# Optimization experiments

Hardware: AMD Instinct MI355X
Metric: run time of the kernel (lower is better)

## Reference

```python
import jax, jax.numpy as jnp
import numpy as np

FEAT = 32          # feat_size
N = FEAT * FEAT    # sequence length = 1024
D = 256            # d_model
DK = 32            # per-head dim (hardcoded in module)
H = D // DK        # num_heads = 8
B = 16
NUM_REL = (2 * FEAT - 1) ** 2


def _rel_index():
    coords = np.stack(np.meshgrid(np.arange(FEAT), np.arange(FEAT), indexing='ij'), axis=-1).reshape(-1, 2)
    rel = coords[:, None, :] - coords[None, :, :]  # [N, N, 2]
    rel += FEAT - 1
    return (rel[..., 0] * (2 * FEAT - 1) + rel[..., 1]).astype(np.int32)  # [N, N]


def setup_inputs() -> dict:
    key = jax.random.key(0)
    ks = jax.random.split(key, 10)
    std = 0.02
    inp = {
        'x': jax.random.normal(ks[0], (B, N, D), jnp.float32),
        'Wq': jax.random.normal(ks[1], (D, D), jnp.float32) * std,
        'bq': jnp.zeros((D,), jnp.float32),
        'Wk': jax.random.normal(ks[2], (D, D), jnp.float32) * std,
        'bk': jnp.zeros((D,), jnp.float32),
        'Wv': jax.random.normal(ks[3], (D, D), jnp.float32) * std,
        'bv': jnp.zeros((D,), jnp.float32),
        'Wo': jax.random.normal(ks[4], (D, D), jnp.float32) * std,
        'bo': jnp.zeros((D,), jnp.float32),
        'bias_table': jax.random.normal(ks[5], (H, NUM_REL), jnp.float32) * std,
        'rel_index': jnp.asarray(_rel_index()),  # [N, N] int32
    }
    return inp


def reference(x, Wq, bq, Wk, bk, Wv, bv, Wo, bo, bias_table, rel_index):
    Bn, Nn, C = x.shape
    # torch Linear: y = x @ W.T + b
    def proj(W, b):
        return (x @ W.T + b).reshape(Bn, Nn, H, DK).transpose(0, 2, 1, 3)  # [B,H,N,dk]
    q, k, v = proj(Wq, bq), proj(Wk, bk), proj(Wv, bv)
    # relative position bias gather: [H, N*N] -> [1,H,N,N]
    rel_bias = bias_table[:, rel_index.reshape(-1)].reshape(1, H, Nn, Nn)
    scale = 1.0 / jnp.sqrt(jnp.float32(DK))
    scores = jnp.einsum('bhqd,bhkd->bhqk', q, k) * scale + rel_bias
    attn = jax.nn.softmax(scores, axis=-1)
    out = jnp.einsum('bhqk,bhkd->bhqd', attn, v)  # [B,H,N,dk]
    out = out.transpose(0, 2, 1, 3).reshape(Bn, Nn, C)
    return out @ Wo.T + bo
```

## Files before the change

### kernel.cpp

```cpp
#include <hip/hip_runtime.h>


typedef unsigned short u16;
typedef unsigned int u32;
typedef short short8 __attribute__((ext_vector_type(8)));
typedef u16 u16x4 __attribute__((ext_vector_type(4)));
typedef u32 u32x2 __attribute__((ext_vector_type(2)));
typedef float f32x4 __attribute__((ext_vector_type(4)));

#define NREL 3969
#define LOG2E 1.4426950408889634f
#define QS2 (0.17677669529663687f * 1.4426950408889634f)

__device__ __forceinline__ u16 f2bf(float f) {
  union { float f; unsigned u; } x; x.f = f;
  unsigned r = x.u + 0x7fffu + ((x.u >> 16) & 1u);
  return (u16)(r >> 16);
}

__device__ __forceinline__ u32 cvt_pk_bf16(float lo, float hi) {
  u32 r;
  asm("v_cvt_pk_bf16_f32 %0, %1, %2" : "=v"(r) : "v"(lo), "v"(hi));
  return r;
}

__device__ __forceinline__ float fast_exp2(float x) {
  float r;
  asm("v_exp_f32 %0, %1" : "=v"(r) : "v"(x));
  return r;
}

__device__ __forceinline__ void glds16(const u16* g, u16* l) {
  __builtin_amdgcn_global_load_lds((const __attribute__((address_space(1))) u32*)g,
                                   (__attribute__((address_space(3))) u32*)l, 16, 0, 0);
}

template <int N> __device__ __forceinline__ void wait_vm() {
  asm volatile("s_waitcnt vmcnt(%0)" ::"n"(N) : "memory");
}

__global__ __launch_bounds__(256) void cast_all_k(
    const float4* __restrict__ x,
    const float* __restrict__ wq, const float* __restrict__ wk,
    const float* __restrict__ wv, const float* __restrict__ wo,
    u16x4* __restrict__ xout, u16x4* __restrict__ wout) {
  int i = blockIdx.x * 256 + threadIdx.x;
  float4 v;
  u16x4* dst;
  if (i < 1048576) {
    v = x[i];
    dst = xout + i;
  } else {
    int wf = i - 1048576;
    int wi = wf >> 14, off = wf & 16383;
    const float* src = (wi == 0) ? wq : (wi == 1) ? wk : (wi == 2) ? wv : wo;
    v = ((const float4*)src)[off];
    dst = wout + wf;
  }
  u16x4 o;
  o[0] = f2bf(v.x); o[1] = f2bf(v.y); o[2] = f2bf(v.z); o[3] = f2bf(v.w);
  *dst = o;
}

__global__ __launch_bounds__(256, 3) void proj_qkv_k(
    const u16* __restrict__ A, const u16* __restrict__ Wc,
    const float* __restrict__ b0, const float* __restrict__ b1,
    const float* __restrict__ b2,
    u16* __restrict__ qb, u16* __restrict__ kb, u16* __restrict__ vtb) {
  const int lid = (blockIdx.x & 7) * 96 + (blockIdx.x >> 3);
  const int m0 = (lid / 6) * 128;
  const int n0 = (lid % 6) * 128;
  __shared__ u16 SH[24576];
  const int tid = threadIdx.x;
  const int wave = tid >> 6, lane = tid & 63;
  const int fr = lane & 15, kg = lane >> 4;
  const int wm = wave >> 1, wn = wave & 1;
  const int l2 = lane >> 2;
  const int sseg = ((lane & 3) ^ (l2 & 3)) * 8;
  const u16* gA = A + (m0 + wave * 16 + l2) * 256 + sseg;
  const u16* gB = Wc + (n0 + wave * 16 + l2) * 256 + sseg;
  const int dstw = wave * 1024;
  const int rsw = (kg * 16) ^ ((fr & 3) << 4);

  f32x4 acc[4][4];
#pragma unroll
  for (int i = 0; i < 4; ++i)
#pragma unroll
    for (int j = 0; j < 4; ++j) acc[i][j] = (f32x4){0.f, 0.f, 0.f, 0.f};

  const int ws = (n0 + wn * 64) >> 8;
  const bool vm = (ws == 2);

#define PSTG(t, sb)                                                     \
  do {                                                                  \
    glds16(gA + (t) * 32,         (u16*)((char*)SH + (sb) + dstw));     \
    glds16(gA + 16384 + (t) * 32, (u16*)((char*)SH + (sb) + 4096 + dstw)); \
    glds16(gB + (t) * 32,         (u16*)((char*)SH + (sb) + 8192 + dstw)); \
    glds16(gB + 16384 + (t) * 32, (u16*)((char*)SH + (sb) + 12288 + dstw)); \
  } while (0)

  PSTG(0, 0);
  PSTG(1, 16384);
#pragma unroll
  for (int it = 0; it < 8; ++it) {
    if (it < 6) PSTG(it + 2, ((it + 2) % 3) * 16384);
    if (it < 6) wait_vm<8>();
    else if (it == 6) wait_vm<4>();
    else wait_vm<0>();
    __builtin_amdgcn_s_barrier();
    const char* abase = (const char*)SH + (it % 3) * 16384;
    const char* bbase = abase + 8192;
    short8 af[4], bf[4];
#pragma unroll
    for (int i = 0; i < 4; ++i) {
      af[i] = *(const short8*)(abase + (wm * 64 + i * 16 + fr) * 64 + rsw);
      bf[i] = *(const short8*)(bbase + (wn * 64 + i * 16 + fr) * 64 + rsw);
    }
    if (vm) {
#pragma unroll
      for (int mi = 0; mi < 4; ++mi)
#pragma unroll
        for (int ni = 0; ni < 4; ++ni)
          acc[mi][ni] = __builtin_amdgcn_mfma_f32_16x16x32_bf16(af[mi], bf[ni], acc[mi][ni], 0, 0, 0);
    } else {
#pragma unroll
      for (int mi = 0; mi < 4; ++mi)
#pragma unroll
        for (int ni = 0; ni < 4; ++ni)
          acc[mi][ni] = __builtin_amdgcn_mfma_f32_16x16x32_bf16(bf[ni], af[mi], acc[mi][ni], 0, 0, 0);
    }
    __builtin_amdgcn_s_barrier();
  }
#undef PSTG

  const int bI = m0 >> 10;
  const int s0 = (m0 & 1023) + wm * 64;
  const int nbb = (n0 + wn * 64) & 255;
  char* shw = (char*)SH + wave * 8192;
  if (vm) {
#pragma unroll
    for (int ni = 0; ni < 4; ++ni) {
      const int nl = ni * 16 + fr;
      const float bias = b2[nbb + nl];
#pragma unroll
      for (int mi = 0; mi < 4; ++mi) {
        u16x4 pk;
#pragma unroll
        for (int r = 0; r < 4; ++r) pk[r] = f2bf(acc[mi][ni][r] + bias);
        *(u16x4*)(shw + nl * 128 + (((mi * 16 + kg * 4) * 2) ^ ((nl & 7) << 4))) = pk;
      }
    }
    const int l8 = lane >> 3, seg8 = lane & 7;
#pragma unroll
    for (int i = 0; i < 8; ++i) {
      const int nl = i * 8 + l8;
      const short8 val = *(const short8*)(shw + nl * 128 + ((seg8 * 16) ^ ((nl & 7) << 4)));
      const int hg = (nbb >> 5) + (nl >> 5), dd = nl & 31;
      *(short8*)(vtb + ((bI * 8 + hg) * 32 + dd) * 1024 + s0 + seg8 * 8) = val;
    }
  } else {
    const float* bp = (ws == 0) ? b0 : b1;
    u16* dst = (ws == 0) ? qb : kb;
    const float sc = (ws == 0) ? QS2 : 1.0f;
#pragma unroll
    for (int ni = 0; ni < 4; ++ni) {
      const float4 b4 = *(const float4*)(bp + nbb + ni * 16 + kg * 4);
#pragma unroll
      for (int mi = 0; mi < 4; ++mi) {
        const int sl = mi * 16 + fr;
        u16x4 pk;
#pragma unroll
        for (int r = 0; r < 4; ++r) pk[r] = f2bf((acc[mi][ni][r] + b4[r]) * sc);
        *(u16x4*)(shw + sl * 128 + (((ni * 32 + kg * 8)) ^ ((sl & 7) << 4))) = pk;
      }
    }
    const int l4 = lane >> 2, seg = lane & 3;
#pragma unroll
    for (int hh = 0; hh < 2; ++hh) {
#pragma unroll
      for (int g = 0; g < 4; ++g) {
        const int sl = g * 16 + l4;
        const short8 val = *(const short8*)(shw + sl * 128 + ((hh * 64 + seg * 16) ^ ((sl & 7) << 4)));
        const int hg = (nbb >> 5) + hh;
        *(short8*)(dst + ((bI * 8 + hg) * 1024 + s0 + sl) * 32 + seg * 8) = val;
      }
    }
  }
}

__global__ __launch_bounds__(256, 4) void proj_out_k(
    const u16* __restrict__ A, const u16* __restrict__ Wc,
    const float* __restrict__ bo, float* __restrict__ outp) {
  const int lid = (blockIdx.x & 7) * 64 + (blockIdx.x >> 3);
  const int m0 = (lid >> 1) * 64;
  const int n0 = (lid & 1) * 128;
  __shared__ u16 SH[18432];
  const int tid = threadIdx.x;
  const int wave = tid >> 6, lane = tid & 63;
  const int fr = lane & 15, kg = lane >> 4;
  const int wm = wave >> 1, wn = wave & 1;
  const int l2 = lane >> 2;
  const int sseg = ((lane & 3) ^ (l2 & 3)) * 8;
  const u16* gA = A + (m0 + wave * 16 + l2) * 256 + sseg;
  const u16* gB = Wc + (768 + n0 + wave * 16 + l2) * 256 + sseg;
  const int dstw = wave * 1024;
  const int rsw = (kg * 16) ^ ((fr & 3) << 4);

  f32x4 acc[2][4];
#pragma unroll
  for (int i = 0; i < 2; ++i)
#pragma unroll
    for (int j = 0; j < 4; ++j) acc[i][j] = (f32x4){0.f, 0.f, 0.f, 0.f};

#define OSTG(t, sb)                                                     \
  do {                                                                  \
    glds16(gA + (t) * 32,         (u16*)((char*)SH + (sb) + dstw));     \
    glds16(gB + (t) * 32,         (u16*)((char*)SH + (sb) + 4096 + dstw)); \
    glds16(gB + 16384 + (t) * 32, (u16*)((char*)SH + (sb) + 8192 + dstw)); \
  } while (0)

  OSTG(0, 0);
  OSTG(1, 12288);
#pragma unroll
  for (int it = 0; it < 8; ++it) {
    if (it < 6) OSTG(it + 2, ((it + 2) % 3) * 12288);
    if (it < 6) wait_vm<6>();
    else if (it == 6) wait_vm<3>();
    else wait_vm<0>();
    __builtin_amdgcn_s_barrier();
    const char* abase = (const char*)SH + (it % 3) * 12288;
    const char* bbase = abase + 4096;
    short8 af[2], bf[4];
#pragma unroll
    for (int i = 0; i < 2; ++i)
      af[i] = *(const short8*)(abase + (wm * 32 + i * 16 + fr) * 64 + rsw);
#pragma unroll
    for (int i = 0; i < 4; ++i)
      bf[i] = *(const short8*)(bbase + (wn * 64 + i * 16 + fr) * 64 + rsw);
#pragma unroll
    for (int mi = 0; mi < 2; ++mi)
#pragma unroll
      for (int ni = 0; ni < 4; ++ni)
        acc[mi][ni] = __builtin_amdgcn_mfma_f32_16x16x32_bf16(bf[ni], af[mi], acc[mi][ni], 0, 0, 0);
    __builtin_amdgcn_s_barrier();
  }
#undef OSTG

#pragma unroll
  for (int ni = 0; ni < 4; ++ni) {
    const int n4 = n0 + wn * 64 + ni * 16 + kg * 4;
    const float4 b4 = *(const float4*)(bo + n4);
#pragma unroll
    for (int mi = 0; mi < 2; ++mi) {
      const int m = m0 + wm * 32 + mi * 16 + fr;
      float4 o;
#pragma unroll
      for (int r = 0; r < 4; ++r) o[r] = acc[mi][ni][r] + b4[r];
      *(float4*)(outp + m * 256 + n4) = o;
    }
  }
}

__global__ __launch_bounds__(256, 5) void rel_attn_k(
    const u16* __restrict__ qb, const u16* __restrict__ kb,
    const u16* __restrict__ vtb, const float* __restrict__ btab,
    u16* __restrict__ ao) {
  const int bid0 = blockIdx.x;
  const int lid = (bid0 & 7) * 256 + (bid0 >> 3);
  const int bh = lid >> 4, qt = lid & 15;
  const int h = bh & 7, b = bh >> 3;
  const int q0 = qt * 64;
  __shared__ u16 bias_lb[3972];
  __shared__ u16 Kl[2][2048];
  __shared__ u16 Vl[2][2048];
  __shared__ u16 Pl[4][1024];
  const int tid = threadIdx.x;
  const int wave = tid >> 6, lane = tid & 63;
  const int fr = lane & 15, kg = lane >> 4;

  for (int i = tid; i < NREL; i += 256) bias_lb[i] = f2bf(btab[h * NREL + i] * LOG2E);

  const int krow = tid >> 2;
  const u16* kgsrc = kb + (bh * 1024 + krow) * 32 + ((tid & 3) ^ (krow & 3)) * 8;
  const int vrow = tid >> 3;
  const u16* vgsrc = vtb + (bh * 32 + vrow) * 1024 + ((tid & 7) ^ (vrow & 7)) * 8;
  u16* kld = &Kl[0][0] + wave * 512;
  u16* vld = &Vl[0][0] + wave * 512;

  const int q = q0 + wave * 16 + fr;
  const short8 qf = *(const short8*)(qb + (bh * 1024 + q) * 32 + kg * 8);
  const int qbase = (q >> 5) * 63 + (q & 31) + 1984;
  char* pw = (char*)Pl[wave] + fr * 128;
  const int swz = (fr & 7) << 4;

  short8 ones;
#pragma unroll
  for (int j = 0; j < 8; ++j) ones[j] = (short)0x3F80;

  f32x4 oacc[2], lacc;
  oacc[0] = (f32x4){0.f, 0.f, 0.f, 0.f};
  oacc[1] = (f32x4){0.f, 0.f, 0.f, 0.f};
  lacc = (f32x4){0.f, 0.f, 0.f, 0.f};

  glds16(kgsrc, kld);
  glds16(vgsrc, vld);
  __syncthreads();

  for (int kt = 0; kt < 16; ++kt) {
    const int cur = kt & 1;
    if (kt < 15) {
      glds16(kgsrc + (kt + 1) * 2048, kld + (cur ^ 1) * 2048);
      glds16(vgsrc + (kt + 1) * 64, vld + (cur ^ 1) * 2048);
      wait_vm<2>();
    } else {
      wait_vm<0>();
    }
    __builtin_amdgcn_s_barrier();

    const char* kbase = (const char*)Kl[cur];
    const char* vbase = (const char*)Vl[cur];
    short8 kf[4], vf[2][2];
#pragma unroll
    for (int g = 0; g < 4; ++g)
      kf[g] = *(const short8*)(kbase + (g * 16 + fr) * 64 + ((kg * 16) ^ ((fr & 3) << 4)));
#pragma unroll
    for (int ks = 0; ks < 2; ++ks)
#pragma unroll
      for (int g2 = 0; g2 < 2; ++g2)
        vf[ks][g2] = *(const short8*)(vbase + (g2 * 16 + fr) * 128 + (((ks * 4 + kg) << 4) ^ swz));

    f32x4 sacc[4];
    __builtin_amdgcn_s_setprio(1);
#pragma unroll
    for (int g = 0; g < 4; ++g)
      sacc[g] = __builtin_amdgcn_mfma_f32_16x16x32_bf16(kf[g], qf, (f32x4){0.f, 0.f, 0.f, 0.f}, 0, 0, 0);
    __builtin_amdgcn_s_setprio(0);

    const int t0 = qbase - kt * 126 - kg * 4;
    u32 pk[4][2];
#pragma unroll
    for (int g = 0; g < 4; ++g) {
      const int ag = t0 - g * 16 - 31 * (g >> 1);
      float e[4];
#pragma unroll
      for (int r = 0; r < 4; ++r) {
        union { u32 u; float f; } bc;
        bc.u = (u32)bias_lb[ag - r] << 16;
        e[r] = fast_exp2(sacc[g][r] + bc.f);
      }
      pk[g][0] = cvt_pk_bf16(e[0], e[1]);
      pk[g][1] = cvt_pk_bf16(e[2], e[3]);
    }

#pragma unroll
    for (int g = 0; g < 4; ++g) {
      u32x2 w2;
      w2[0] = pk[g][0];
      w2[1] = pk[g][1];
      *(u32x2*)(pw + ((g * 32 + kg * 8) ^ swz)) = w2;
    }

#pragma unroll
    for (int ks = 0; ks < 2; ++ks) {
      const short8 pf = *(const short8*)(pw + ((ks * 64 + kg * 16) ^ swz));
      __builtin_amdgcn_s_setprio(1);
      oacc[0] = __builtin_amdgcn_mfma_f32_16x16x32_bf16(pf, vf[ks][0], oacc[0], 0, 0, 0);
      oacc[1] = __builtin_amdgcn_mfma_f32_16x16x32_bf16(pf, vf[ks][1], oacc[1], 0, 0, 0);
      lacc = __builtin_amdgcn_mfma_f32_16x16x32_bf16(pf, ones, lacc, 0, 0, 0);
      __builtin_amdgcn_s_setprio(0);
    }
    __builtin_amdgcn_s_barrier();
  }

#pragma unroll
  for (int r = 0; r < 4; ++r) {
    const float inv = __builtin_amdgcn_rcpf(lacc[r]);
#pragma unroll
    for (int g2 = 0; g2 < 2; ++g2)
      *(u16*)((char*)Pl[wave] + (kg * 4 + r) * 64 + (g2 * 16 + fr) * 2) =
          f2bf(oacc[g2][r] * inv);
  }
  const int orow = lane >> 2, oseg = lane & 3;
  const short8 ov = *(const short8*)((char*)Pl[wave] + orow * 64 + oseg * 16);
  *(short8*)(ao + (b * 1024 + q0 + wave * 16 + orow) * 256 + h * 32 + oseg * 8) = ov;
}

extern "C" void kernel_launch(void* const* d_in, const int* in_sizes, int n_in,
                              void* d_out, int out_size, void* d_ws, size_t ws_size,
                              hipStream_t stream) {
  (void)in_sizes; (void)n_in; (void)out_size; (void)ws_size;
  const float* x    = (const float*)d_in[0];
  const float* Wq   = (const float*)d_in[1];
  const float* bq   = (const float*)d_in[2];
  const float* Wk   = (const float*)d_in[3];
  const float* bk   = (const float*)d_in[4];
  const float* Wv   = (const float*)d_in[5];
  const float* bv   = (const float*)d_in[6];
  const float* Wo   = (const float*)d_in[7];
  const float* bo   = (const float*)d_in[8];
  const float* btab = (const float*)d_in[9];
  float* out = (float*)d_out;
  char* ws = (char*)d_ws;

  u16* xbf  = (u16*)(ws + 0);
  u16* Wcat = (u16*)(ws + 8388608);
  u16* qbuf = (u16*)(ws + 8912896);
  u16* kbuf = (u16*)(ws + 17301504);
  u16* vtb  = (u16*)(ws + 25690112);

  cast_all_k<<<4352, 256, 0, stream>>>((const float4*)x, Wq, Wk, Wv, Wo,
                                       (u16x4*)xbf, (u16x4*)Wcat);
  proj_qkv_k<<<768, 256, 0, stream>>>(xbf, Wcat, bq, bk, bv, qbuf, kbuf, vtb);
  rel_attn_k<<<2048, 256, 0, stream>>>(qbuf, kbuf, vtb, btab, xbf);
  proj_out_k<<<512, 256, 0, stream>>>(xbf, Wcat, bo, out);
}
```

Measured before the change: 158.6 us.

## Fuse fp32-to-bf16 cast of x into QKV projection GEMM loads

The separate cast kernel now converts only the weights. The QKV projection reads fp32 x directly, converts it to bf16 in registers and stores it swizzled into LDS, so the bf16 copy of x is no longer written to and read back from HBM. Both projection GEMMs also move from a 3-stage async pipeline to a 2-stage double buffer with __syncthreads, which frees LDS for higher occupancy (launch bound 3→4 for QKV). In exchange the main loop loads A through registers synchronously, which can expose more latency, and the 6 column tiles per row block each re-read fp32 x, which is twice the bytes of bf16.

```diff
diff --git a/kernel.cpp b/kernel.cpp
--- a/kernel.cpp
+++ b/kernel.cpp
@@ -6,6 +6,7 @@
 typedef short short8 __attribute__((ext_vector_type(8)));
 typedef u16 u16x4 __attribute__((ext_vector_type(4)));
 typedef u32 u32x2 __attribute__((ext_vector_type(2)));
+typedef u32 u32x4 __attribute__((ext_vector_type(4)));
 typedef float f32x4 __attribute__((ext_vector_type(4)));
 
 #define NREL 3969
@@ -39,47 +40,39 @@
   asm volatile("s_waitcnt vmcnt(%0)" ::"n"(N) : "memory");
 }
 
-__global__ __launch_bounds__(256) void cast_all_k(
-    const float4* __restrict__ x,
+__global__ __launch_bounds__(256) void cast_w_k(
     const float* __restrict__ wq, const float* __restrict__ wk,
     const float* __restrict__ wv, const float* __restrict__ wo,
-    u16x4* __restrict__ xout, u16x4* __restrict__ wout) {
+    u16x4* __restrict__ wout) {
   int i = blockIdx.x * 256 + threadIdx.x;
-  float4 v;
-  u16x4* dst;
-  if (i < 1048576) {
-    v = x[i];
-    dst = xout + i;
-  } else {
-    int wf = i - 1048576;
-    int wi = wf >> 14, off = wf & 16383;
-    const float* src = (wi == 0) ? wq : (wi == 1) ? wk : (wi == 2) ? wv : wo;
-    v = ((const float4*)src)[off];
-    dst = wout + wf;
-  }
+  int wi = i >> 14, off = i & 16383;
+  const float* src = (wi == 0) ? wq : (wi == 1) ? wk : (wi == 2) ? wv : wo;
+  float4 v = ((const float4*)src)[off];
   u16x4 o;
   o[0] = f2bf(v.x); o[1] = f2bf(v.y); o[2] = f2bf(v.z); o[3] = f2bf(v.w);
-  *dst = o;
-}
-
-__global__ __launch_bounds__(256, 3) void proj_qkv_k(
-    const u16* __restrict__ A, const u16* __restrict__ Wc,
+  wout[i] = o;
+}
+
+__global__ __launch_bounds__(256, 4) void proj_qkv_k(
+    const float* __restrict__ X, const u16* __restrict__ Wc,
     const float* __restrict__ b0, const float* __restrict__ b1,
     const float* __restrict__ b2,
     u16* __restrict__ qb, u16* __restrict__ kb, u16* __restrict__ vtb) {
   const int lid = (blockIdx.x & 7) * 96 + (blockIdx.x >> 3);
   const int m0 = (lid / 6) * 128;
   const int n0 = (lid % 6) * 128;
-  __shared__ u16 SH[24576];
+  __shared__ u16 SH[16384];
   const int tid = threadIdx.x;
   const int wave = tid >> 6, lane = tid & 63;
   const int fr = lane & 15, kg = lane >> 4;
   const int wm = wave >> 1, wn = wave & 1;
   const int l2 = lane >> 2;
   const int sseg = ((lane & 3) ^ (l2 & 3)) * 8;
-  const u16* gA = A + (m0 + wave * 16 + l2) * 256 + sseg;
   const u16* gB = Wc + (n0 + wave * 16 + l2) * 256 + sseg;
-  const int dstw = wave * 1024;
+  const float* gX = X + (m0 + (tid >> 1)) * 256 + (tid & 1) * 16;
+  const int arow = tid >> 1, acg = tid & 1;
+  const int aw0 = arow * 64 + ((acg * 32) ^ ((arow & 3) << 4));
+  const int aw1 = arow * 64 + ((acg * 32 + 16) ^ ((arow & 3) << 4));
   const int rsw = (kg * 16) ^ ((fr & 3) << 4);
 
   f32x4 acc[4][4];
@@ -91,24 +84,33 @@
   const int ws = (n0 + wn * 64) >> 8;
   const bool vm = (ws == 2);
 
-#define PSTG(t, sb)                                                     \
-  do {                                                                  \
-    glds16(gA + (t) * 32,         (u16*)((char*)SH + (sb) + dstw));     \
-    glds16(gA + 16384 + (t) * 32, (u16*)((char*)SH + (sb) + 4096 + dstw)); \
-    glds16(gB + (t) * 32,         (u16*)((char*)SH + (sb) + 8192 + dstw)); \
-    glds16(gB + 16384 + (t) * 32, (u16*)((char*)SH + (sb) + 12288 + dstw)); \
-  } while (0)
-
-  PSTG(0, 0);
-  PSTG(1, 16384);
-#pragma unroll
+  float4 ar[4];
+#pragma unroll
+  for (int q = 0; q < 4; ++q) ar[q] = *(const float4*)(gX + q * 4);
+  glds16(gB, (u16*)((char*)SH + 8192 + wave * 1024));
+  glds16(gB + 16384, (u16*)((char*)SH + 12288 + wave * 1024));
+  {
+    u32x4 w0, w1;
+    w0[0] = cvt_pk_bf16(ar[0][0], ar[0][1]); w0[1] = cvt_pk_bf16(ar[0][2], ar[0][3]);
+    w0[2] = cvt_pk_bf16(ar[1][0], ar[1][1]); w0[3] = cvt_pk_bf16(ar[1][2], ar[1][3]);
+    w1[0] = cvt_pk_bf16(ar[2][0], ar[2][1]); w1[1] = cvt_pk_bf16(ar[2][2], ar[2][3]);
+    w1[2] = cvt_pk_bf16(ar[3][0], ar[3][1]); w1[3] = cvt_pk_bf16(ar[3][2], ar[3][3]);
+    *(u32x4*)((char*)SH + aw0) = w0;
+    *(u32x4*)((char*)SH + aw1) = w1;
+  }
+  __syncthreads();
+
   for (int it = 0; it < 8; ++it) {
-    if (it < 6) PSTG(it + 2, ((it + 2) % 3) * 16384);
-    if (it < 6) wait_vm<8>();
-    else if (it == 6) wait_vm<4>();
-    else wait_vm<0>();
-    __builtin_amdgcn_s_barrier();
-    const char* abase = (const char*)SH + (it % 3) * 16384;
+    const int cb = (it & 1) ? 16384 : 0;
+    const int nb = 16384 - cb;
+    if (it < 7) {
+      const int ko = (it + 1) * 32;
+#pragma unroll
+      for (int q = 0; q < 4; ++q) ar[q] = *(const float4*)(gX + ko + q * 4);
+      glds16(gB + ko, (u16*)((char*)SH + nb + 8192 + wave * 1024));
+      glds16(gB + 16384 + ko, (u16*)((char*)SH + nb + 12288 + wave * 1024));
+    }
+    const char* abase = (const char*)SH + cb;
     const char* bbase = abase + 8192;
     short8 af[4], bf[4];
 #pragma unroll
@@ -129,9 +131,17 @@
         for (int ni = 0; ni < 4; ++ni)
           acc[mi][ni] = __builtin_amdgcn_mfma_f32_16x16x32_bf16(bf[ni], af[mi], acc[mi][ni], 0, 0, 0);
     }
-    __builtin_amdgcn_s_barrier();
-  }
-#undef PSTG
+    if (it < 7) {
+      u32x4 w0, w1;
+      w0[0] = cvt_pk_bf16(ar[0][0], ar[0][1]); w0[1] = cvt_pk_bf16(ar[0][2], ar[0][3]);
+      w0[2] = cvt_pk_bf16(ar[1][0], ar[1][1]); w0[3] = cvt_pk_bf16(ar[1][2], ar[1][3]);
+      w1[0] = cvt_pk_bf16(ar[2][0], ar[2][1]); w1[1] = cvt_pk_bf16(ar[2][2], ar[2][3]);
+      w1[2] = cvt_pk_bf16(ar[3][0], ar[3][1]); w1[3] = cvt_pk_bf16(ar[3][2], ar[3][3]);
+      *(u32x4*)((char*)SH + nb + aw0) = w0;
+      *(u32x4*)((char*)SH + nb + aw1) = w1;
+    }
+    __syncthreads();
+  }
 
   const int bI = m0 >> 10;
   const int s0 = (m0 & 1023) + wm * 64;
@@ -194,7 +204,7 @@
   const int lid = (blockIdx.x & 7) * 64 + (blockIdx.x >> 3);
   const int m0 = (lid >> 1) * 64;
   const int n0 = (lid & 1) * 128;
-  __shared__ u16 SH[18432];
+  __shared__ u16 SH[12288];
   const int tid = threadIdx.x;
   const int wave = tid >> 6, lane = tid & 63;
   const int fr = lane & 15, kg = lane >> 4;
@@ -203,7 +213,6 @@
   const int sseg = ((lane & 3) ^ (l2 & 3)) * 8;
   const u16* gA = A + (m0 + wave * 16 + l2) * 256 + sseg;
   const u16* gB = Wc + (768 + n0 + wave * 16 + l2) * 256 + sseg;
-  const int dstw = wave * 1024;
   const int rsw = (kg * 16) ^ ((fr & 3) << 4);
 
   f32x4 acc[2][4];
@@ -212,23 +221,20 @@
 #pragma unroll
     for (int j = 0; j < 4; ++j) acc[i][j] = (f32x4){0.f, 0.f, 0.f, 0.f};
 
-#define OSTG(t, sb)                                                     \
-  do {                                                                  \
-    glds16(gA + (t) * 32,         (u16*)((char*)SH + (sb) + dstw));     \
-    glds16(gB + (t) * 32,         (u16*)((char*)SH + (sb) + 4096 + dstw)); \
-    glds16(gB + 16384 + (t) * 32, (u16*)((char*)SH + (sb) + 8192 + dstw)); \
+#define OSTG(t, sb)                                                        \
+  do {                                                                     \
+    glds16(gA + (t) * 32,         (u16*)((char*)SH + (sb) + wave * 1024)); \
+    glds16(gB + (t) * 32,         (u16*)((char*)SH + (sb) + 4096 + wave * 1024)); \
+    glds16(gB + 16384 + (t) * 32, (u16*)((char*)SH + (sb) + 8192 + wave * 1024)); \
   } while (0)
 
   OSTG(0, 0);
-  OSTG(1, 12288);
-#pragma unroll
+  __syncthreads();
   for (int it = 0; it < 8; ++it) {
-    if (it < 6) OSTG(it + 2, ((it + 2) % 3) * 12288);
-    if (it < 6) wait_vm<6>();
-    else if (it == 6) wait_vm<3>();
-    else wait_vm<0>();
-    __builtin_amdgcn_s_barrier();
-    const char* abase = (const char*)SH + (it % 3) * 12288;
+    const int cb = (it & 1) ? 12288 : 0;
+    const int nb = 12288 - cb;
+    if (it < 7) OSTG(it + 1, nb);
+    const char* abase = (const char*)SH + cb;
     const char* bbase = abase + 4096;
     short8 af[2], bf[4];
 #pragma unroll
@@ -242,7 +248,7 @@
 #pragma unroll
       for (int ni = 0; ni < 4; ++ni)
         acc[mi][ni] = __builtin_amdgcn_mfma_f32_16x16x32_bf16(bf[ni], af[mi], acc[mi][ni], 0, 0, 0);
-    __builtin_amdgcn_s_barrier();
+    __syncthreads();
   }
 #undef OSTG
 
@@ -402,15 +408,14 @@
   float* out = (float*)d_out;
   char* ws = (char*)d_ws;
 
-  u16* xbf  = (u16*)(ws + 0);
+  u16* abf  = (u16*)(ws + 0);
   u16* Wcat = (u16*)(ws + 8388608);
   u16* qbuf = (u16*)(ws + 8912896);
   u16* kbuf = (u16*)(ws + 17301504);
   u16* vtb  = (u16*)(ws + 25690112);
 
-  cast_all_k<<<4352, 256, 0, stream>>>((const float4*)x, Wq, Wk, Wv, Wo,
-                                       (u16x4*)xbf, (u16x4*)Wcat);
-  proj_qkv_k<<<768, 256, 0, stream>>>(xbf, Wcat, bq, bk, bv, qbuf, kbuf, vtb);
-  rel_attn_k<<<2048, 256, 0, stream>>>(qbuf, kbuf, vtb, btab, xbf);
-  proj_out_k<<<512, 256, 0, stream>>>(xbf, Wcat, bo, out);
-}
+  cast_w_k<<<256, 256, 0, stream>>>(Wq, Wk, Wv, Wo, (u16x4*)Wcat);
+  proj_qkv_k<<<768, 256, 0, stream>>>(x, Wcat, bq, bk, bv, qbuf, kbuf, vtb);
+  rel_attn_k<<<2048, 256, 0, stream>>>(qbuf, kbuf, vtb, btab, abf);
+  proj_out_k<<<512, 256, 0, stream>>>(abf, Wcat, bo, out);
+}
```

After: 224.5 us. +41.6%, slower.

## Process two query tiles per attention block to reuse K/V loads

Applied to the files above, without the earlier changes.

Each attention block now handles 128 query rows (two 64-row sub-tiles per wave) instead of 64, halving the grid to 1024 blocks. K/V tiles and the per-head bias table loaded into LDS are reused across both sub-tiles, which halves global K/V traffic and the bias table setup per query. The cost is more live registers (two sets of accumulators and Q fragments), possibly lower occupancy, and fewer blocks for load balancing.

```diff
diff --git a/kernel.cpp b/kernel.cpp
--- a/kernel.cpp
+++ b/kernel.cpp
@@ -266,10 +266,10 @@
     const u16* __restrict__ vtb, const float* __restrict__ btab,
     u16* __restrict__ ao) {
   const int bid0 = blockIdx.x;
-  const int lid = (bid0 & 7) * 256 + (bid0 >> 3);
-  const int bh = lid >> 4, qt = lid & 15;
+  const int lid = (bid0 & 7) * 128 + (bid0 >> 3);
+  const int bh = lid >> 3, qp = lid & 7;
   const int h = bh & 7, b = bh >> 3;
-  const int q0 = qt * 64;
+  const int q0 = qp * 128;
   __shared__ u16 bias_lb[3972];
   __shared__ u16 Kl[2][2048];
   __shared__ u16 Vl[2][2048];
@@ -287,9 +287,11 @@
   u16* kld = &Kl[0][0] + wave * 512;
   u16* vld = &Vl[0][0] + wave * 512;
 
-  const int q = q0 + wave * 16 + fr;
-  const short8 qf = *(const short8*)(qb + (bh * 1024 + q) * 32 + kg * 8);
-  const int qbase = (q >> 5) * 63 + (q & 31) + 1984;
+  const int qA = q0 + wave * 16 + fr;
+  const short8 qfA = *(const short8*)(qb + (bh * 1024 + qA) * 32 + kg * 8);
+  const short8 qfB = *(const short8*)(qb + (bh * 1024 + qA + 64) * 32 + kg * 8);
+  const int qbaseA = (qA >> 5) * 63 + (qA & 31) + 1984;
+  const int qbaseB = qbaseA + 126;
   char* pw = (char*)Pl[wave] + fr * 128;
   const int swz = (fr & 7) << 4;
 
@@ -297,10 +299,13 @@
 #pragma unroll
   for (int j = 0; j < 8; ++j) ones[j] = (short)0x3F80;
 
-  f32x4 oacc[2], lacc;
-  oacc[0] = (f32x4){0.f, 0.f, 0.f, 0.f};
-  oacc[1] = (f32x4){0.f, 0.f, 0.f, 0.f};
-  lacc = (f32x4){0.f, 0.f, 0.f, 0.f};
+  f32x4 oaccA[2], oaccB[2], laccA, laccB;
+  oaccA[0] = (f32x4){0.f, 0.f, 0.f, 0.f};
+  oaccA[1] = (f32x4){0.f, 0.f, 0.f, 0.f};
+  oaccB[0] = (f32x4){0.f, 0.f, 0.f, 0.f};
+  oaccB[1] = (f32x4){0.f, 0.f, 0.f, 0.f};
+  laccA = (f32x4){0.f, 0.f, 0.f, 0.f};
+  laccB = (f32x4){0.f, 0.f, 0.f, 0.f};
 
   glds16(kgsrc, kld);
   glds16(vgsrc, vld);
@@ -329,60 +334,115 @@
       for (int g2 = 0; g2 < 2; ++g2)
         vf[ks][g2] = *(const short8*)(vbase + (g2 * 16 + fr) * 128 + (((ks * 4 + kg) << 4) ^ swz));
 
-    f32x4 sacc[4];
-    __builtin_amdgcn_s_setprio(1);
-#pragma unroll
-    for (int g = 0; g < 4; ++g)
-      sacc[g] = __builtin_amdgcn_mfma_f32_16x16x32_bf16(kf[g], qf, (f32x4){0.f, 0.f, 0.f, 0.f}, 0, 0, 0);
-    __builtin_amdgcn_s_setprio(0);
-
-    const int t0 = qbase - kt * 126 - kg * 4;
-    u32 pk[4][2];
-#pragma unroll
-    for (int g = 0; g < 4; ++g) {
-      const int ag = t0 - g * 16 - 31 * (g >> 1);
-      float e[4];
-#pragma unroll
-      for (int r = 0; r < 4; ++r) {
-        union { u32 u; float f; } bc;
-        bc.u = (u32)bias_lb[ag - r] << 16;
-        e[r] = fast_exp2(sacc[g][r] + bc.f);
-      }
-      pk[g][0] = cvt_pk_bf16(e[0], e[1]);
-      pk[g][1] = cvt_pk_bf16(e[2], e[3]);
-    }
-
-#pragma unroll
-    for (int g = 0; g < 4; ++g) {
-      u32x2 w2;
-      w2[0] = pk[g][0];
-      w2[1] = pk[g][1];
-      *(u32x2*)(pw + ((g * 32 + kg * 8) ^ swz)) = w2;
-    }
-
-#pragma unroll
-    for (int ks = 0; ks < 2; ++ks) {
-      const short8 pf = *(const short8*)(pw + ((ks * 64 + kg * 16) ^ swz));
+    const int t0k = -kt * 126 - kg * 4;
+
+    {
+      f32x4 sacc[4];
       __builtin_amdgcn_s_setprio(1);
-      oacc[0] = __builtin_amdgcn_mfma_f32_16x16x32_bf16(pf, vf[ks][0], oacc[0], 0, 0, 0);
-      oacc[1] = __builtin_amdgcn_mfma_f32_16x16x32_bf16(pf, vf[ks][1], oacc[1], 0, 0, 0);
-      lacc = __builtin_amdgcn_mfma_f32_16x16x32_bf16(pf, ones, lacc, 0, 0, 0);
+#pragma unroll
+      for (int g = 0; g < 4; ++g)
+        sacc[g] = __builtin_amdgcn_mfma_f32_16x16x32_bf16(kf[g], qfA, (f32x4){0.f, 0.f, 0.f, 0.f}, 0, 0, 0);
       __builtin_amdgcn_s_setprio(0);
-    }
-    __builtin_amdgcn_s_barrier();
-  }
-
+      const int t0 = qbaseA + t0k;
+      u32 pk[4][2];
+#pragma unroll
+      for (int g = 0; g < 4; ++g) {
+        const int ag = t0 - g * 16 - 31 * (g >> 1);
+        float e[4];
+#pragma unroll
+        for (int r = 0; r < 4; ++r) {
+          union { u32 u; float f; } bc;
+          bc.u = (u32)bias_lb[ag - r] << 16;
+          e[r] = fast_exp2(sacc[g][r] + bc.f);
+        }
+        pk[g][0] = cvt_pk_bf16(e[0], e[1]);
+        pk[g][1] = cvt_pk_bf16(e[2], e[3]);
+      }
+#pragma unroll
+      for (int g = 0; g < 4; ++g) {
+        u32x2 w2;
+        w2[0] = pk[g][0];
+        w2[1] = pk[g][1];
+        *(u32x2*)(pw + ((g * 32 + kg * 8) ^ swz)) = w2;
+      }
+#pragma unroll
+      for (int ks = 0; ks < 2; ++ks) {
+        const short8 pf = *(const short8*)(pw + ((ks * 64 + kg * 16) ^ swz));
+        __builtin_amdgcn_s_setprio(1);
+        oaccA[0] = __builtin_amdgcn_mfma_f32_16x16x32_bf16(pf, vf[ks][0], oaccA[0], 0, 0, 0);
+        oaccA[1] = __builtin_amdgcn_mfma_f32_16x16x32_bf16(pf, vf[ks][1], oaccA[1], 0, 0, 0);
+        laccA = __builtin_amdgcn_mfma_f32_16x16x32_bf16(pf, ones, laccA, 0, 0, 0);
+        __builtin_amdgcn_s_setprio(0);
+      }
+    }
+
+    {
+      f32x4 sacc[4];
+      __builtin_amdgcn_s_setprio(1);
+#pragma unroll
+      for (int g = 0; g < 4; ++g)
+        sacc[g] = __builtin_amdgcn_mfma_f32_16x16x32_bf16(kf[g], qfB, (f32x4){0.f, 0.f, 0.f, 0.f}, 0, 0, 0);
+      __builtin_amdgcn_s_setprio(0);
+      const int t0 = qbaseB + t0k;
+      u32 pk[4][2];
+#pragma unroll
+      for (int g = 0; g < 4; ++g) {
+        const int ag = t0 - g * 16 - 31 * (g >> 1);
+        float e[4];
+#pragma unroll
+        for (int r = 0; r < 4; ++r) {
+          union { u32 u; float f; } bc;
+          bc.u = (u32)bias_lb[ag - r] << 16;
+          e[r] = fast_exp2(sacc[g][r] + bc.f);
+        }
+        pk[g][0] = cvt_pk_bf16(e[0], e[1]);
+        pk[g][1] = cvt_pk_bf16(e[2], e[3]);
+      }
+#pragma unroll
+      for (int g = 0; g < 4; ++g) {
+        u32x2 w2;
+        w2[0] = pk[g][0];
+        w2[1] = pk[g][1];
+        *(u32x2*)(pw + ((g * 32 + kg * 8) ^ swz)) = w2;
+      }
+#pragma unroll
+      for (int ks = 0; ks < 2; ++ks) {
+        const short8 pf = *(const short8*)(pw + ((ks * 64 + kg * 16) ^ swz));
+        __builtin_amdgcn_s_setprio(1);
+        oaccB[0] = __builtin_amdgcn_mfma_f32_16x16x32_bf16(pf, vf[ks][0], oaccB[0], 0, 0, 0);
+        oaccB[1] = __builtin_amdgcn_mfma_f32_16x16x32_bf16(pf, vf[ks][1], oaccB[1], 0, 0, 0);
+        laccB = __builtin_amdgcn_mfma_f32_16x16x32_bf16(pf, ones, laccB, 0, 0, 0);
+        __builtin_amdgcn_s_setprio(0);
+      }
+    }
+    __builtin_amdgcn_s_barrier();
+  }
+
+  const int orow = lane >> 2, oseg = lane & 3;
 #pragma unroll
   for (int r = 0; r < 4; ++r) {
-    const float inv = __builtin_amdgcn_rcpf(lacc[r]);
+    const float inv = __builtin_amdgcn_rcpf(laccA[r]);
 #pragma unroll
     for (int g2 = 0; g2 < 2; ++g2)
       *(u16*)((char*)Pl[wave] + (kg * 4 + r) * 64 + (g2 * 16 + fr) * 2) =
-          f2bf(oacc[g2][r] * inv);
-  }
-  const int orow = lane >> 2, oseg = lane & 3;
-  const short8 ov = *(const short8*)((char*)Pl[wave] + orow * 64 + oseg * 16);
-  *(short8*)(ao + (b * 1024 + q0 + wave * 16 + orow) * 256 + h * 32 + oseg * 8) = ov;
+          f2bf(oaccA[g2][r] * inv);
+  }
+  {
+    const short8 ov = *(const short8*)((char*)Pl[wave] + orow * 64 + oseg * 16);
+    *(short8*)(ao + (b * 1024 + q0 + wave * 16 + orow) * 256 + h * 32 + oseg * 8) = ov;
+  }
+#pragma unroll
+  for (int r = 0; r < 4; ++r) {
+    const float inv = __builtin_amdgcn_rcpf(laccB[r]);
+#pragma unroll
+    for (int g2 = 0; g2 < 2; ++g2)
+      *(u16*)((char*)Pl[wave] + (kg * 4 + r) * 64 + (g2 * 16 + fr) * 2) =
+          f2bf(oaccB[g2][r] * inv);
+  }
+  {
+    const short8 ov = *(const short8*)((char*)Pl[wave] + orow * 64 + oseg * 16);
+    *(short8*)(ao + (b * 1024 + q0 + 64 + wave * 16 + orow) * 256 + h * 32 + oseg * 8) = ov;
+  }
 }
 
 extern "C" void kernel_launch(void* const* d_in, const int* in_sizes, int n_in,
@@ -411,6 +471,6 @@
   cast_all_k<<<4352, 256, 0, stream>>>((const float4*)x, Wq, Wk, Wv, Wo,
                                        (u16x4*)xbf, (u16x4*)Wcat);
   proj_qkv_k<<<768, 256, 0, stream>>>(xbf, Wcat, bq, bk, bv, qbuf, kbuf, vtb);
-  rel_attn_k<<<2048, 256, 0, stream>>>(qbuf, kbuf, vtb, btab, xbf);
+  rel_attn_k<<<1024, 256, 0, stream>>>(qbuf, kbuf, vtb, btab, xbf);
   proj_out_k<<<512, 256, 0, stream>>>(xbf, Wcat, bo, out);
 }
```

Measured after the change: 166.0 us. 1.05x slower.

## Load K/V fragments directly from global into registers, dropping LDS staging

Applied to the files above, without the earlier changes.

The attention kernel no longer stages K and V tiles through double-buffered shared memory with per-tile barriers. Each wave now loads its MFMA fragments straight from global memory into registers, ping-ponging between two register sets so the next tile's loads overlap the current tile's compute. This removes the LDS traffic and the block-wide barriers, but each of the four waves now fetches the same K/V data separately (more global/L2 traffic) and register pressure rises. The occupancy hint is lowered from 5 to 4 blocks to make room for the extra registers.

```diff
diff --git a/kernel.cpp b/kernel.cpp
--- a/kernel.cpp
+++ b/kernel.cpp
@@ -261,7 +261,7 @@
   }
 }
 
-__global__ __launch_bounds__(256, 5) void rel_attn_k(
+__global__ __launch_bounds__(256, 4) void rel_attn_k(
     const u16* __restrict__ qb, const u16* __restrict__ kb,
     const u16* __restrict__ vtb, const float* __restrict__ btab,
     u16* __restrict__ ao) {
@@ -271,8 +271,6 @@
   const int h = bh & 7, b = bh >> 3;
   const int q0 = qt * 64;
   __shared__ u16 bias_lb[3972];
-  __shared__ u16 Kl[2][2048];
-  __shared__ u16 Vl[2][2048];
   __shared__ u16 Pl[4][1024];
   const int tid = threadIdx.x;
   const int wave = tid >> 6, lane = tid & 63;
@@ -280,16 +278,11 @@
 
   for (int i = tid; i < NREL; i += 256) bias_lb[i] = f2bf(btab[h * NREL + i] * LOG2E);
 
-  const int krow = tid >> 2;
-  const u16* kgsrc = kb + (bh * 1024 + krow) * 32 + ((tid & 3) ^ (krow & 3)) * 8;
-  const int vrow = tid >> 3;
-  const u16* vgsrc = vtb + (bh * 32 + vrow) * 1024 + ((tid & 7) ^ (vrow & 7)) * 8;
-  u16* kld = &Kl[0][0] + wave * 512;
-  u16* vld = &Vl[0][0] + wave * 512;
-
   const int q = q0 + wave * 16 + fr;
   const short8 qf = *(const short8*)(qb + (bh * 1024 + q) * 32 + kg * 8);
   const int qbase = (q >> 5) * 63 + (q & 31) + 1984;
+  const u16* kp = kb + (bh * 1024 + fr) * 32 + kg * 8;
+  const u16* vp = vtb + (bh * 32 + fr) * 1024 + kg * 8;
   char* pw = (char*)Pl[wave] + fr * 128;
   const int swz = (fr & 7) << 4;
 
@@ -302,75 +295,80 @@
   oacc[1] = (f32x4){0.f, 0.f, 0.f, 0.f};
   lacc = (f32x4){0.f, 0.f, 0.f, 0.f};
 
-  glds16(kgsrc, kld);
-  glds16(vgsrc, vld);
   __syncthreads();
 
-  for (int kt = 0; kt < 16; ++kt) {
-    const int cur = kt & 1;
-    if (kt < 15) {
-      glds16(kgsrc + (kt + 1) * 2048, kld + (cur ^ 1) * 2048);
-      glds16(vgsrc + (kt + 1) * 64, vld + (cur ^ 1) * 2048);
-      wait_vm<2>();
-    } else {
-      wait_vm<0>();
-    }
-    __builtin_amdgcn_s_barrier();
-
-    const char* kbase = (const char*)Kl[cur];
-    const char* vbase = (const char*)Vl[cur];
-    short8 kf[4], vf[2][2];
-#pragma unroll
-    for (int g = 0; g < 4; ++g)
-      kf[g] = *(const short8*)(kbase + (g * 16 + fr) * 64 + ((kg * 16) ^ ((fr & 3) << 4)));
-#pragma unroll
-    for (int ks = 0; ks < 2; ++ks)
-#pragma unroll
-      for (int g2 = 0; g2 < 2; ++g2)
-        vf[ks][g2] = *(const short8*)(vbase + (g2 * 16 + fr) * 128 + (((ks * 4 + kg) << 4) ^ swz));
-
-    f32x4 sacc[4];
-    __builtin_amdgcn_s_setprio(1);
-#pragma unroll
-    for (int g = 0; g < 4; ++g)
-      sacc[g] = __builtin_amdgcn_mfma_f32_16x16x32_bf16(kf[g], qf, (f32x4){0.f, 0.f, 0.f, 0.f}, 0, 0, 0);
-    __builtin_amdgcn_s_setprio(0);
-
-    const int t0 = qbase - kt * 126 - kg * 4;
-    u32 pk[4][2];
-#pragma unroll
-    for (int g = 0; g < 4; ++g) {
-      const int ag = t0 - g * 16 - 31 * (g >> 1);
-      float e[4];
-#pragma unroll
-      for (int r = 0; r < 4; ++r) {
-        union { u32 u; float f; } bc;
-        bc.u = (u32)bias_lb[ag - r] << 16;
-        e[r] = fast_exp2(sacc[g][r] + bc.f);
-      }
-      pk[g][0] = cvt_pk_bf16(e[0], e[1]);
-      pk[g][1] = cvt_pk_bf16(e[2], e[3]);
-    }
-
-#pragma unroll
-    for (int g = 0; g < 4; ++g) {
-      u32x2 w2;
-      w2[0] = pk[g][0];
-      w2[1] = pk[g][1];
-      *(u32x2*)(pw + ((g * 32 + kg * 8) ^ swz)) = w2;
-    }
-
-#pragma unroll
-    for (int ks = 0; ks < 2; ++ks) {
-      const short8 pf = *(const short8*)(pw + ((ks * 64 + kg * 16) ^ swz));
-      __builtin_amdgcn_s_setprio(1);
-      oacc[0] = __builtin_amdgcn_mfma_f32_16x16x32_bf16(pf, vf[ks][0], oacc[0], 0, 0, 0);
-      oacc[1] = __builtin_amdgcn_mfma_f32_16x16x32_bf16(pf, vf[ks][1], oacc[1], 0, 0, 0);
-      lacc = __builtin_amdgcn_mfma_f32_16x16x32_bf16(pf, ones, lacc, 0, 0, 0);
-      __builtin_amdgcn_s_setprio(0);
-    }
-    __builtin_amdgcn_s_barrier();
-  }
+#define LOADK(dst, t)                                                  \
+  do {                                                                 \
+    _Pragma("unroll")                                                  \
+    for (int g = 0; g < 4; ++g)                                        \
+      dst[g] = *(const short8*)(kp + (t) * 2048 + g * 512);            \
+  } while (0)
+#define LOADV(dst, t)                                                  \
+  do {                                                                 \
+    _Pragma("unroll")                                                  \
+    for (int ks = 0; ks < 2; ++ks)                                     \
+      _Pragma("unroll")                                                \
+      for (int g2 = 0; g2 < 2; ++g2)                                   \
+        dst[ks][g2] = *(const short8*)(vp + g2 * 16384 + (t) * 64 + ks * 32); \
+  } while (0)
+#define COMPUTE(t, kf, vf)                                             \
+  do {                                                                 \
+    f32x4 sacc[4];                                                     \
+    __builtin_amdgcn_s_setprio(1);                                     \
+    _Pragma("unroll")                                                  \
+    for (int g = 0; g < 4; ++g)                                        \
+      sacc[g] = __builtin_amdgcn_mfma_f32_16x16x32_bf16(kf[g], qf, (f32x4){0.f, 0.f, 0.f, 0.f}, 0, 0, 0); \
+    __builtin_amdgcn_s_setprio(0);                                     \
+    const int tt = qbase - (t) * 126 - kg * 4;                         \
+    u32 pk2[4][2];                                                     \
+    _Pragma("unroll")                                                  \
+    for (int g = 0; g < 4; ++g) {                                      \
+      const int ag = tt - g * 16 - 31 * (g >> 1);                      \
+      float e[4];                                                      \
+      _Pragma("unroll")                                                \
+      for (int r = 0; r < 4; ++r) {                                    \
+        union { u32 u; float f; } bc;                                  \
+        bc.u = (u32)bias_lb[ag - r] << 16;                             \
+        e[r] = fast_exp2(sacc[g][r] + bc.f);                           \
+      }                                                                \
+      pk2[g][0] = cvt_pk_bf16(e[0], e[1]);                             \
+      pk2[g][1] = cvt_pk_bf16(e[2], e[3]);                             \
+    }                                                                  \
+    _Pragma("unroll")                                                  \
+    for (int g = 0; g < 4; ++g) {                                      \
+      u32x2 w2;                                                        \
+      w2[0] = pk2[g][0];                                               \
+      w2[1] = pk2[g][1];                                               \
+      *(u32x2*)(pw + ((g * 32 + kg * 8) ^ swz)) = w2;                  \
+    }                                                                  \
+    _Pragma("unroll")                                                  \
+    for (int ks = 0; ks < 2; ++ks) {                                   \
+      const short8 pf = *(const short8*)(pw + ((ks * 64 + kg * 16) ^ swz)); \
+      __builtin_amdgcn_s_setprio(1);                                   \
+      oacc[0] = __builtin_amdgcn_mfma_f32_16x16x32_bf16(pf, vf[ks][0], oacc[0], 0, 0, 0); \
+      oacc[1] = __builtin_amdgcn_mfma_f32_16x16x32_bf16(pf, vf[ks][1], oacc[1], 0, 0, 0); \
+      lacc = __builtin_amdgcn_mfma_f32_16x16x32_bf16(pf, ones, lacc, 0, 0, 0); \
+      __builtin_amdgcn_s_setprio(0);                                   \
+    }                                                                  \
+  } while (0)
+
+  short8 kA[4], kB[4], vA[2][2], vB[2][2];
+  LOADK(kA, 0);
+  LOADV(vA, 0);
+#pragma unroll 1
+  for (int kt2 = 0; kt2 < 8; ++kt2) {
+    const int t0 = kt2 * 2;
+    LOADK(kB, t0 + 1);
+    LOADV(vB, t0 + 1);
+    COMPUTE(t0, kA, vA);
+    const int t2 = (t0 + 2 < 16) ? (t0 + 2) : 15;
+    LOADK(kA, t2);
+    LOADV(vA, t2);
+    COMPUTE(t0 + 1, kB, vB);
+  }
+#undef LOADK
+#undef LOADV
+#undef COMPUTE
 
 #pragma unroll
   for (int r = 0; r < 4; ++r) {
```

Result: slower. 204.2 us (+28.7%).
